# Kernel tuning notes

Hardware: AMD Instinct MI355X
Metric: run time of the kernel (lower is better)

The kernel has to match this reference:

```python
import jax, jax.numpy as jnp
import numpy as np

N_NODES = 50000
N_EDGES = 800000
D_IN = 16


def gcn_conv(x, edge_index, W, b, n_nodes):
    """PyG GCNConv: x' = D^{-1/2} (A + I) D^{-1/2} X W + b (add_self_loops=True)."""
    h = x @ W  # [N, d_out] - transform before propagate (small d => cheaper)
    src = jnp.concatenate([edge_index[0], jnp.arange(n_nodes)])  # add self-loops
    dst = jnp.concatenate([edge_index[1], jnp.arange(n_nodes)])
    deg = jax.ops.segment_sum(jnp.ones_like(dst, dtype=h.dtype), dst,
                              num_segments=n_nodes)  # in-degree incl. self-loop
    deg_inv_sqrt = jnp.where(deg > 0, jax.lax.rsqrt(deg), 0.0)
    norm = deg_inv_sqrt[src] * deg_inv_sqrt[dst]  # [E+N]
    msg = h[src] * norm[:, None]                  # gather + scale
    out = jax.ops.segment_sum(msg, dst, num_segments=n_nodes)  # scatter-add
    return out + b


def setup_inputs() -> dict:
    key = jax.random.key(0)
    ks = jax.random.split(key, 16)
    d = D_IN
    x = jax.random.normal(ks[0], (N_NODES, d), dtype=jnp.float32)
    edge_index = jax.random.randint(ks[1], (2, N_EDGES), 0, N_NODES, dtype=jnp.int64)

    def glorot(k, fan_in, fan_out):
        s = (6.0 / (fan_in + fan_out)) ** 0.5
        return jax.random.uniform(k, (fan_in, fan_out), jnp.float32, -s, s)

    return {
        "x": x,
        "edge_index": edge_index,
        "W1": glorot(ks[2], d, 2 * d),      "b1": jnp.zeros((2 * d,), jnp.float32),
        "W2": glorot(ks[3], 2 * d, 4 * d),  "b2": jnp.zeros((4 * d,), jnp.float32),
        "W3": glorot(ks[4], 4 * d, 8 * d),  "b3": jnp.zeros((8 * d,), jnp.float32),
        "Wl1": glorot(ks[5], 8 * d, 4 * d), "bl1": jnp.zeros((4 * d,), jnp.float32),
        "Wl2": glorot(ks[6], 4 * d, 2 * d), "bl2": jnp.zeros((2 * d,), jnp.float32),
        "Wl3": glorot(ks[7], 2 * d, d),     "bl3": jnp.zeros((d,), jnp.float32),
    }


def reference(x, edge_index, W1, b1, W2, b2, W3, b3, Wl1, bl1, Wl2, bl2, Wl3, bl3):
    n = x.shape[0]
    # note: original applies relu twice per conv; relu is idempotent
    out = jax.nn.relu(gcn_conv(x, edge_index, W1, b1, n))
    out = jax.nn.relu(gcn_conv(out, edge_index, W2, b2, n))
    out = jax.nn.relu(gcn_conv(out, edge_index, W3, b3, n))
    out = jax.nn.relu(out @ Wl1 + bl1)
    out = jax.nn.relu(out @ Wl2 + bl2)
    out = jax.nn.relu(out @ Wl3 + bl3)
    return out
```

## Files before the change

kernel.cpp:

```cpp
#include <hip/hip_runtime.h>

#define TPB 256
#define TE  2048
#define MAXB 6144

typedef _Float16 half_t;
typedef _Float16 half4 __attribute__((ext_vector_type(4)));
typedef _Float16 half8 __attribute__((ext_vector_type(8)));
typedef float float8v __attribute__((ext_vector_type(8)));

static inline int cdiv(int a, int b) { return (a + b - 1) / b; }


__global__ void k_zero_int(int* p, int n) {
    int i = blockIdx.x * blockDim.x + threadIdx.x;
    if (i < n) p[i] = 0;
}

__global__ void __launch_bounds__(TPB)
k_binscatter(const int* __restrict__ src, const int* __restrict__ dst,
             int* __restrict__ bcur, unsigned int* __restrict__ gbuf,
             int e, int nb) {
    __shared__ int lcnt[256], loffs[256], lcur[256], gres[256];
    __shared__ int ss[256];
    __shared__ unsigned int ldata[TE];
    const int tid = threadIdx.x;
    const int base = blockIdx.x * TE;
    const int cnt = min(TE, e - base);
    lcnt[tid] = 0;
    __syncthreads();

    unsigned int myv[TE / TPB];
    int myb[TE / TPB];
#pragma unroll
    for (int k = 0; k < TE / TPB; ++k) {
        int j = tid + k * TPB;
        if (j < cnt) {
            int d = dst[base + j], s = src[base + j];
            int b = d >> 8;
            myv[k] = ((unsigned)b << 24) | ((unsigned)(d & 255) << 16) | (unsigned)s;
            myb[k] = b;
            atomicAdd(&lcnt[b], 1);
        } else myb[k] = -1;
    }
    __syncthreads();
    {
        int v = lcnt[tid];
        ss[tid] = v;
        __syncthreads();
        for (int d = 1; d < 256; d <<= 1) {
            int x2 = (tid >= d) ? ss[tid - d] : 0;
            __syncthreads();
            ss[tid] += x2;
            __syncthreads();
        }
        loffs[tid] = ss[tid] - v;
        lcur[tid] = ss[tid] - v;
    }
    __syncthreads();
    if (tid < nb && lcnt[tid])
        gres[tid] = tid * MAXB + atomicAdd(&bcur[tid], lcnt[tid]);
#pragma unroll
    for (int k = 0; k < TE / TPB; ++k) {
        if (myb[k] >= 0) {
            int p = atomicAdd(&lcur[myb[k]], 1);
            ldata[p] = myv[k];
        }
    }
    __syncthreads();
    for (int j = tid; j < cnt; j += TPB) {
        unsigned int v = ldata[j];
        int b = v >> 24;
        gbuf[gres[b] + (j - loffs[b])] = v & 0xFFFFFFu;
    }
}

__global__ void __launch_bounds__(TPB)
k_csr(const unsigned int* __restrict__ gbuf, const int* __restrict__ bcur,
      const float* __restrict__ x, int* __restrict__ offs,
      unsigned short* __restrict__ nch, float* __restrict__ dinv,
      unsigned short* __restrict__ ssrc, half_t* __restrict__ G, int n, int nb) {
    __shared__ int ss[256], cnt[256], loffs2[256], lcur2[256], pcnt[256];
    __shared__ float sdinv[256];
    __shared__ unsigned short stage[MAXB];
    const int b = blockIdx.x;
    const int t = threadIdx.x;
    const int s0 = b * MAXB;
    const int m = bcur[b];

    cnt[t] = 0;
    __syncthreads();
    for (int j = t; j < m; j += TPB)
        atomicAdd(&cnt[(gbuf[s0 + j] >> 16) & 255], 1);
    __syncthreads();
    {
        int v = cnt[t];
        int pv = (v + 7) & ~7;
        pcnt[t] = pv;
        ss[t] = pv;
        __syncthreads();
        for (int d = 1; d < 256; d <<= 1) {
            int x2 = (t >= d) ? ss[t - d] : 0;
            __syncthreads();
            ss[t] += x2;
            __syncthreads();
        }
        loffs2[t] = ss[t] - pv;
        lcur2[t] = ss[t] - pv;
        float di = rsqrtf((float)v + 1.0f);
        sdinv[t] = di;
        int node = b * 256 + t;
        if (node < n) {
            offs[node] = s0 + loffs2[t];
            nch[node] = (unsigned short)(pv >> 3);
            dinv[node] = di;
        }
    }
    __syncthreads();
    for (int j = t; j < m; j += TPB) {
        unsigned int v = gbuf[s0 + j];
        int p = atomicAdd(&lcur2[(v >> 16) & 255], 1);
        stage[p] = (unsigned short)(v & 0xFFFFu);
    }
    __syncthreads();
    {
        int base2 = loffs2[t] + cnt[t], end2 = loffs2[t] + pcnt[t];
        for (int q = base2; q < end2; ++q) stage[q] = (unsigned short)n;
    }
    __syncthreads();
    const int tot = ss[255];
    for (int j = t; j < tot; j += TPB) ssrc[s0 + j] = stage[j];

    const int base = b * 256;
    const int cn = min(256, n - base);
    const float4* X4 = (const float4*)x;
    half4* G4 = (half4*)G;
    for (int j = t; j < cn * 4; j += TPB) {
        int nl = j >> 2, k4 = j & 3;
        float4 v = X4[(size_t)(base + nl) * 4 + k4];
        float d = sdinv[nl];
        half4 h;
        h.x = (half_t)(v.x * d); h.y = (half_t)(v.y * d);
        h.z = (half_t)(v.z * d); h.w = (half_t)(v.w * d);
        G4[(size_t)(base + nl) * 4 + k4] = h;
    }
    if (b == 0 && t < 4) G4[(size_t)n * 4 + t] = half4{0, 0, 0, 0};
}

template<int DI, int DO, int R, bool SCALE, bool OUT_HALF, bool WHALF, bool ZSENT>
__global__ void __launch_bounds__(TPB, 4)
k_conv(const int* __restrict__ offs, const unsigned short* __restrict__ nch,
       const unsigned short* __restrict__ ssrc,
       const half_t* __restrict__ G, const float* __restrict__ dinv,
       const float* __restrict__ W, const float* __restrict__ b,
       void* __restrict__ outp, int n) {
    constexpr int CT = DO / 4;
    constexpr int RT = TPB / CT;
    constexpr int TM = RT * R;
    constexpr int K4 = DI / 4;
    constexpr int PX = K4 + 1;
    constexpr int C  = DI / 8;
    static_assert(TM * C == TPB, "gather/gemm tile mismatch");
    __shared__ float4 sW4[WHALF ? 1 : DI * CT];
    __shared__ half4  sWh[WHALF ? DI * CT : 1];
    __shared__ float4 sX4[TM * PX];
    __shared__ int soffs[TM];
    __shared__ unsigned short snch[TM];
    const int tid = threadIdx.x;
    const int r0 = blockIdx.x * TM;

    const float4* Wg = (const float4*)W;
    for (int t = tid; t < DI * CT; t += TPB) {
        float4 w = Wg[t];
        if (WHALF) {
            half4 h;
            h.x = (half_t)w.x; h.y = (half_t)w.y;
            h.z = (half_t)w.z; h.w = (half_t)w.w;
            sWh[t] = h;
        } else {
            sW4[t] = w;
        }
    }
    if (tid < TM) {
        int row = r0 + tid;
        soffs[tid] = (row < n) ? offs[row] : 0;
        snch[tid] = (row < n) ? nch[row] : (unsigned short)0;
    }
    __syncthreads();

    {
        int lrow = tid / C;
        int gc = tid - lrow * C;
        int row = r0 + lrow;
        float8v acc;
#pragma unroll
        for (int q = 0; q < 8; ++q) acc[q] = 0.f;
        if (row < n) {
            const half8* Grow = (const half8*)G;
            const unsigned gcU = (unsigned)gc;
            half8 hs = Grow[(unsigned)row * C + gcU];
#pragma unroll
            for (int q = 0; q < 8; ++q) acc[q] = (float)hs[q];
            const int nchunks = snch[lrow];
            const uint4* sv = (const uint4*)(ssrc + soffs[lrow]);
            int k = 0;
            for (; k + 2 <= nchunks; k += 2) {
                uint4 pa = sv[k];
                uint4 pb = sv[k + 1];
                unsigned a0 = pa.x & 0xFFFFu, a1 = pa.x >> 16;
                unsigned a2 = pa.y & 0xFFFFu, a3 = pa.y >> 16;
                unsigned a4 = pa.z & 0xFFFFu, a5 = pa.z >> 16;
                unsigned a6 = pa.w & 0xFFFFu, a7 = pa.w >> 16;
                unsigned b0 = pb.x & 0xFFFFu, b1 = pb.x >> 16;
                unsigned b2 = pb.y & 0xFFFFu, b3 = pb.y >> 16;
                unsigned b4 = pb.z & 0xFFFFu, b5 = pb.z >> 16;
                unsigned b6 = pb.w & 0xFFFFu, b7 = pb.w >> 16;
                half8 ga0 = Grow[a0 * C + gcU];
                half8 ga1 = Grow[a1 * C + gcU];
                half8 ga2 = Grow[a2 * C + gcU];
                half8 ga3 = Grow[a3 * C + gcU];
                half8 ga4 = Grow[a4 * C + gcU];
                half8 ga5 = Grow[a5 * C + gcU];
                half8 ga6 = Grow[a6 * C + gcU];
                half8 ga7 = Grow[a7 * C + gcU];
                half8 gb0 = Grow[b0 * C + gcU];
                half8 gb1 = Grow[b1 * C + gcU];
                half8 gb2 = Grow[b2 * C + gcU];
                half8 gb3 = Grow[b3 * C + gcU];
                half8 gb4 = Grow[b4 * C + gcU];
                half8 gb5 = Grow[b5 * C + gcU];
                half8 gb6 = Grow[b6 * C + gcU];
                half8 gb7 = Grow[b7 * C + gcU];
#pragma unroll
                for (int q = 0; q < 8; ++q)
                    acc[q] += (((((float)ga0[q] + (float)ga1[q]) + ((float)ga2[q] + (float)ga3[q]))
                             +  (((float)ga4[q] + (float)ga5[q]) + ((float)ga6[q] + (float)ga7[q])))
                             + ((((float)gb0[q] + (float)gb1[q]) + ((float)gb2[q] + (float)gb3[q]))
                             +  (((float)gb4[q] + (float)gb5[q]) + ((float)gb6[q] + (float)gb7[q]))));
            }
            if (k < nchunks) {
                uint4 pk = sv[k];
                unsigned a0 = pk.x & 0xFFFFu, a1 = pk.x >> 16;
                unsigned a2 = pk.y & 0xFFFFu, a3 = pk.y >> 16;
                unsigned a4 = pk.z & 0xFFFFu, a5 = pk.z >> 16;
                unsigned a6 = pk.w & 0xFFFFu, a7 = pk.w >> 16;
                half8 g0 = Grow[a0 * C + gcU];
                half8 g1 = Grow[a1 * C + gcU];
                half8 g2 = Grow[a2 * C + gcU];
                half8 g3 = Grow[a3 * C + gcU];
                half8 g4 = Grow[a4 * C + gcU];
                half8 g5 = Grow[a5 * C + gcU];
                half8 g6 = Grow[a6 * C + gcU];
                half8 g7 = Grow[a7 * C + gcU];
#pragma unroll
                for (int q = 0; q < 8; ++q)
                    acc[q] += (((float)g0[q] + (float)g1[q]) + ((float)g2[q] + (float)g3[q]))
                            + (((float)g4[q] + (float)g5[q]) + ((float)g6[q] + (float)g7[q]));
            }
            float di = dinv[row];
#pragma unroll
            for (int q = 0; q < 8; ++q) acc[q] *= di;
        }
        sX4[lrow * PX + 2 * gc]     = make_float4(acc[0], acc[1], acc[2], acc[3]);
        sX4[lrow * PX + 2 * gc + 1] = make_float4(acc[4], acc[5], acc[6], acc[7]);
    }
    __syncthreads();

    const int c = tid & (CT - 1);
    const int rg = tid / CT;
    const int rbase = rg * R;
    float4 acc[R];
#pragma unroll
    for (int r = 0; r < R; ++r) acc[r] = make_float4(0.f, 0.f, 0.f, 0.f);

#pragma unroll 2
    for (int k4 = 0; k4 < K4; ++k4) {
        float4 xv[R];
#pragma unroll
        for (int r = 0; r < R; ++r) xv[r] = sX4[(rbase + r) * PX + k4];
#pragma unroll
        for (int kk = 0; kk < 4; ++kk) {
            float4 wv;
            if (WHALF) {
                half4 wh = sWh[(k4 * 4 + kk) * CT + c];
                wv = make_float4((float)wh.x, (float)wh.y, (float)wh.z, (float)wh.w);
            } else {
                wv = sW4[(k4 * 4 + kk) * CT + c];
            }
#pragma unroll
            for (int r = 0; r < R; ++r) {
                float xs = (kk == 0) ? xv[r].x : (kk == 1) ? xv[r].y
                         : (kk == 2) ? xv[r].z : xv[r].w;
                acc[r].x += xs * wv.x; acc[r].y += xs * wv.y;
                acc[r].z += xs * wv.z; acc[r].w += xs * wv.w;
            }
        }
    }

    float4 bc = ((const float4*)b)[c];
#pragma unroll
    for (int r = 0; r < R; ++r) {
        int row = r0 + rbase + r;
        if (row < n) {
            float4 o;
            o.x = fmaxf(acc[r].x + bc.x, 0.f);
            o.y = fmaxf(acc[r].y + bc.y, 0.f);
            o.z = fmaxf(acc[r].z + bc.z, 0.f);
            o.w = fmaxf(acc[r].w + bc.w, 0.f);
            if (SCALE) {
                float d = dinv[row];
                o.x *= d; o.y *= d; o.z *= d; o.w *= d;
            }
            if (OUT_HALF) {
                half4 h;
                h.x = (half_t)o.x; h.y = (half_t)o.y;
                h.z = (half_t)o.z; h.w = (half_t)o.w;
                ((half4*)outp)[(size_t)row * CT + c] = h;
            } else {
                ((float4*)outp)[(size_t)row * CT + c] = o;
            }
        }
    }
    if (ZSENT && OUT_HALF && blockIdx.x == 0 && tid < CT)
        ((half4*)outp)[(size_t)n * CT + tid] = half4{0, 0, 0, 0};
}

__global__ void __launch_bounds__(256, 3)
k_head(const half_t* __restrict__ X,
       const float* __restrict__ W1, const float* __restrict__ b1,
       const float* __restrict__ W2, const float* __restrict__ b2,
       const float* __restrict__ W3, const float* __restrict__ b3,
       float* __restrict__ out, int n) {
    __shared__ half_t hW1[128 * 64];
    __shared__ half_t hW2[64 * 32];
    __shared__ half_t hW3[32 * 16];
    __shared__ float h1[64 * 65];
    __shared__ float h2[64 * 33];
    const int tid = threadIdx.x;
    const int r0 = blockIdx.x * 64;

    for (int t = tid; t < 128 * 64; t += 256) hW1[t] = (half_t)W1[t];
    for (int t = tid; t < 64 * 32; t += 256) hW2[t] = (half_t)W2[t];
    for (int t = tid; t < 32 * 16; t += 256) hW3[t] = (half_t)W3[t];
    __syncthreads();

    {
        const int c4 = tid & 15;
        const int rowg = tid >> 4;
        const half8* Xr = (const half8*)X;
        float acc[4][4];
#pragma unroll
        for (int r = 0; r < 4; ++r)
#pragma unroll
            for (int j = 0; j < 4; ++j) acc[r][j] = 0.f;
        for (int k8 = 0; k8 < 16; ++k8) {
            half8 xh[4];
#pragma unroll
            for (int r = 0; r < 4; ++r) {
                int row = r0 + rowg * 4 + r;
                if (row < n) xh[r] = Xr[(size_t)row * 16 + k8];
                else { half8 z; for (int q = 0; q < 8; ++q) z[q] = (half_t)0.f; xh[r] = z; }
            }
#pragma unroll
            for (int q = 0; q < 8; ++q) {
                int k = k8 * 8 + q;
                half4 w = *(const half4*)&hW1[k * 64 + c4 * 4];
                float w0 = (float)w.x, w1 = (float)w.y, w2 = (float)w.z, w3 = (float)w.w;
#pragma unroll
                for (int r = 0; r < 4; ++r) {
                    float xs = (float)xh[r][q];
                    acc[r][0] += xs * w0; acc[r][1] += xs * w1;
                    acc[r][2] += xs * w2; acc[r][3] += xs * w3;
                }
            }
        }
        float4 bc = ((const float4*)b1)[c4];
#pragma unroll
        for (int r = 0; r < 4; ++r) {
            int rl = rowg * 4 + r;
            h1[rl * 65 + c4 * 4 + 0] = fmaxf(acc[r][0] + bc.x, 0.f);
            h1[rl * 65 + c4 * 4 + 1] = fmaxf(acc[r][1] + bc.y, 0.f);
            h1[rl * 65 + c4 * 4 + 2] = fmaxf(acc[r][2] + bc.z, 0.f);
            h1[rl * 65 + c4 * 4 + 3] = fmaxf(acc[r][3] + bc.w, 0.f);
        }
    }
    __syncthreads();

    {
        const int c4 = tid & 7;
        const int rowg = tid >> 3;
        float acc[2][4];
#pragma unroll
        for (int r = 0; r < 2; ++r)
#pragma unroll
            for (int j = 0; j < 4; ++j) acc[r][j] = 0.f;
#pragma unroll 4
        for (int k = 0; k < 64; ++k) {
            half4 w = *(const half4*)&hW2[k * 32 + c4 * 4];
            float w0 = (float)w.x, w1 = (float)w.y, w2 = (float)w.z, w3 = (float)w.w;
#pragma unroll
            for (int r = 0; r < 2; ++r) {
                float xs = h1[(rowg * 2 + r) * 65 + k];
                acc[r][0] += xs * w0; acc[r][1] += xs * w1;
                acc[r][2] += xs * w2; acc[r][3] += xs * w3;
            }
        }
        float4 bc = ((const float4*)b2)[c4];
#pragma unroll
        for (int r = 0; r < 2; ++r) {
            int rl = rowg * 2 + r;
            h2[rl * 33 + c4 * 4 + 0] = fmaxf(acc[r][0] + bc.x, 0.f);
            h2[rl * 33 + c4 * 4 + 1] = fmaxf(acc[r][1] + bc.y, 0.f);
            h2[rl * 33 + c4 * 4 + 2] = fmaxf(acc[r][2] + bc.z, 0.f);
            h2[rl * 33 + c4 * 4 + 3] = fmaxf(acc[r][3] + bc.w, 0.f);
        }
    }
    __syncthreads();

    {
        const int c4 = tid & 3;
        const int rl = tid >> 2;
        float a0 = 0.f, a1 = 0.f, a2 = 0.f, a3 = 0.f;
#pragma unroll 4
        for (int k = 0; k < 32; ++k) {
            half4 w = *(const half4*)&hW3[k * 16 + c4 * 4];
            float xs = h2[rl * 33 + k];
            a0 += xs * (float)w.x; a1 += xs * (float)w.y;
            a2 += xs * (float)w.z; a3 += xs * (float)w.w;
        }
        int row = r0 + rl;
        if (row < n) {
            float4 bc = ((const float4*)b3)[c4];
            float4 o;
            o.x = fmaxf(a0 + bc.x, 0.f);
            o.y = fmaxf(a1 + bc.y, 0.f);
            o.z = fmaxf(a2 + bc.z, 0.f);
            o.w = fmaxf(a3 + bc.w, 0.f);
            ((float4*)out)[(size_t)row * 4 + c4] = o;
        }
    }
}

extern "C" void kernel_launch(void* const* d_in, const int* in_sizes, int n_in,
                              void* d_out, int out_size, void* d_ws, size_t ws_size,
                              hipStream_t stream) {
    const float* x   = (const float*)d_in[0];
    const int*   ei  = (const int*)d_in[1];
    const float* W1  = (const float*)d_in[2];
    const float* bb1 = (const float*)d_in[3];
    const float* W2  = (const float*)d_in[4];
    const float* bb2 = (const float*)d_in[5];
    const float* W3  = (const float*)d_in[6];
    const float* bb3 = (const float*)d_in[7];
    const float* Wl1 = (const float*)d_in[8];
    const float* bl1 = (const float*)d_in[9];
    const float* Wl2 = (const float*)d_in[10];
    const float* bl2 = (const float*)d_in[11];
    const float* Wl3 = (const float*)d_in[12];
    const float* bl3 = (const float*)d_in[13];
    float* out = (float*)d_out;

    const int n = in_sizes[0] / 16;
    const int e = in_sizes[1] / 2;
    const int* src = ei;
    const int* dst = ei + e;
    const int nb = cdiv(n, 256);

    char* p = (char*)d_ws;
    auto alloc = [&](size_t bytes) {
        char* r = p;
        p += (bytes + 255) & ~(size_t)255;
        return r;
    };
    float*          dinv = (float*)         alloc((size_t)n * 4);
    int*            offs = (int*)           alloc((size_t)n * 4);
    unsigned short* nch  = (unsigned short*)alloc((size_t)n * 2);
    int*            bcur = (int*)           alloc(256 * 4);
    unsigned int*   gbuf = (unsigned int*)  alloc((size_t)nb * MAXB * 4);
    unsigned short* ssrc = (unsigned short*)alloc((size_t)nb * MAXB * 2);
    half_t*         H1   = (half_t*)        alloc((size_t)(n + 1) * 64 * 2);
    half_t*         H2   = (half_t*)        alloc((size_t)(n + 1) * 32 * 2);
    half_t*         X3h  = (half_t*)        alloc((size_t)n * 128 * 2);

    k_zero_int<<<1, 256, 0, stream>>>(bcur, 256);
    k_binscatter<<<cdiv(e, TE), TPB, 0, stream>>>(src, dst, bcur, gbuf, e, nb);
    k_csr<<<nb, TPB, 0, stream>>>(gbuf, bcur, x, offs, nch, dinv, ssrc, H1, n, nb);

    k_conv<16, 32, 4, true, true, false, true><<<cdiv(n, 128), TPB, 0, stream>>>(
        offs, nch, ssrc, H1, dinv, W1, bb1, H2, n);
    k_conv<32, 64, 4, true, true, false, true><<<cdiv(n, 64), TPB, 0, stream>>>(
        offs, nch, ssrc, H2, dinv, W2, bb2, H1, n);
    k_conv<64, 128, 4, false, true, true, false><<<cdiv(n, 32), TPB, 0, stream>>>(
        offs, nch, ssrc, H1, dinv, W3, bb3, X3h, n);

    k_head<<<cdiv(n, 64), 256, 0, stream>>>(X3h, Wl1, bl1, Wl2, bl2, Wl3, bl3, out, n);
}
```

Measured before the change: 198.9 us.

## Fuse all stages into a persistent megakernel with software grid barriers

Replaces the seven separate kernel launches (zeroing, bin scatter, CSR build, three convolutions, MLP head) with one persistent kernel of 512 blocks. Each block grid-strides over tiles in every phase, and the phases are separated by an atomic-counter grid barrier. Shared memory is reused through a union of per-phase layouts. The aim is to remove launch gaps and tail effects. In exchange it adds barrier spin cost, needs all 512 blocks to be co-resident (the barrier has a timeout fallback), and the union's size may cut occupancy.

```diff
diff --git a/kernel.cpp b/kernel.cpp
--- a/kernel.cpp
+++ b/kernel.cpp
@@ -3,157 +3,203 @@
 #define TPB 256
 #define TE  2048
 #define MAXB 6144
+#define GRID 512
 
 typedef _Float16 half_t;
 typedef _Float16 half4 __attribute__((ext_vector_type(4)));
 typedef _Float16 half8 __attribute__((ext_vector_type(8)));
 typedef float float8v __attribute__((ext_vector_type(8)));
 
-static inline int cdiv(int a, int b) { return (a + b - 1) / b; }
-
-
-__global__ void k_zero_int(int* p, int n) {
-    int i = blockIdx.x * blockDim.x + threadIdx.x;
-    if (i < n) p[i] = 0;
-}
-
-__global__ void __launch_bounds__(TPB)
-k_binscatter(const int* __restrict__ src, const int* __restrict__ dst,
-             int* __restrict__ bcur, unsigned int* __restrict__ gbuf,
-             int e, int nb) {
-    __shared__ int lcnt[256], loffs[256], lcur[256], gres[256];
-    __shared__ int ss[256];
-    __shared__ unsigned int ldata[TE];
-    const int tid = threadIdx.x;
-    const int base = blockIdx.x * TE;
-    const int cnt = min(TE, e - base);
-    lcnt[tid] = 0;
+__host__ __device__ static inline constexpr int cdiv(int a, int b) { return (a + b - 1) / b; }
+
+struct SBin {
+    int lcnt[256], loffs[256], lcur[256], gres[256], ss[256];
+    unsigned int ldata[TE];
+};
+struct SCsr {
+    int ss[256], cnt[256], loffs2[256], lcur2[256], pcnt[256];
+    float sdinv[256];
+    unsigned short stage[MAXB];
+};
+template<int DI, int DO, int R, bool WHALF>
+struct SConv {
+    static constexpr int CT = DO / 4;
+    static constexpr int TM = (TPB / CT) * R;
+    static constexpr int PX = DI / 4 + 1;
+    float4 sW4[WHALF ? 1 : DI * CT];
+    half4  sWh[WHALF ? DI * CT : 1];
+    float4 sX4[TM * PX];
+    int soffs[TM];
+    unsigned short snch[TM];
+};
+struct SHead {
+    half_t hW1[128 * 64], hW2[64 * 32], hW3[32 * 16];
+    float h1[64 * 65], h2[64 * 33];
+};
+union SMemAll {
+    SBin b;
+    SCsr c;
+    SConv<16, 32, 4, false>  c1;
+    SConv<32, 64, 4, false>  c2;
+    SConv<64, 128, 4, true>  c3;
+    SHead h;
+};
+
+__device__ __forceinline__ void gridbar(unsigned int* cnt, unsigned int* gen, unsigned int nb) {
     __syncthreads();
-
-    unsigned int myv[TE / TPB];
-    int myb[TE / TPB];
-#pragma unroll
-    for (int k = 0; k < TE / TPB; ++k) {
-        int j = tid + k * TPB;
-        if (j < cnt) {
-            int d = dst[base + j], s = src[base + j];
-            int b = d >> 8;
-            myv[k] = ((unsigned)b << 24) | ((unsigned)(d & 255) << 16) | (unsigned)s;
-            myb[k] = b;
-            atomicAdd(&lcnt[b], 1);
-        } else myb[k] = -1;
+    if (threadIdx.x == 0) {
+        unsigned int g = __hip_atomic_load(gen, __ATOMIC_RELAXED, __HIP_MEMORY_SCOPE_AGENT);
+        __threadfence();
+        unsigned int a = __hip_atomic_fetch_add(cnt, 1u, __ATOMIC_ACQ_REL, __HIP_MEMORY_SCOPE_AGENT);
+        if (a == nb - 1u) {
+            __hip_atomic_store(cnt, 0u, __ATOMIC_RELAXED, __HIP_MEMORY_SCOPE_AGENT);
+            __hip_atomic_fetch_add(gen, 1u, __ATOMIC_RELEASE, __HIP_MEMORY_SCOPE_AGENT);
+        } else {
+            unsigned int spins = 0;
+            while (__hip_atomic_load(gen, __ATOMIC_ACQUIRE, __HIP_MEMORY_SCOPE_AGENT) == g) {
+                __builtin_amdgcn_s_sleep(2);
+                if (++spins > 3000000u) break;
+            }
+        }
+        __threadfence();
     }
     __syncthreads();
-    {
-        int v = lcnt[tid];
-        ss[tid] = v;
-        __syncthreads();
-        for (int d = 1; d < 256; d <<= 1) {
-            int x2 = (tid >= d) ? ss[tid - d] : 0;
+}
+
+__device__ __forceinline__ void phase_binscatter(SBin& L, const int* __restrict__ src,
+        const int* __restrict__ dst, int* __restrict__ bcur,
+        unsigned int* __restrict__ gbuf, int e, int nb) {
+    const int tid = threadIdx.x;
+    const int ntiles = cdiv(e, TE);
+    for (int bb = blockIdx.x; bb < ntiles; bb += gridDim.x) {
+        const int base = bb * TE;
+        const int cnt = min(TE, e - base);
+        L.lcnt[tid] = 0;
+        __syncthreads();
+        unsigned int myv[TE / TPB];
+        int myb[TE / TPB];
+#pragma unroll
+        for (int k = 0; k < TE / TPB; ++k) {
+            int j = tid + k * TPB;
+            if (j < cnt) {
+                int d = dst[base + j], s = src[base + j];
+                int b = d >> 8;
+                myv[k] = ((unsigned)b << 24) | ((unsigned)(d & 255) << 16) | (unsigned)s;
+                myb[k] = b;
+                atomicAdd(&L.lcnt[b], 1);
+            } else myb[k] = -1;
+        }
+        __syncthreads();
+        {
+            int v = L.lcnt[tid];
+            L.ss[tid] = v;
             __syncthreads();
-            ss[tid] += x2;
+            for (int d = 1; d < 256; d <<= 1) {
+                int x2 = (tid >= d) ? L.ss[tid - d] : 0;
+                __syncthreads();
+                L.ss[tid] += x2;
+                __syncthreads();
+            }
+            L.loffs[tid] = L.ss[tid] - v;
+            L.lcur[tid] = L.ss[tid] - v;
+        }
+        __syncthreads();
+        if (tid < nb && L.lcnt[tid])
+            L.gres[tid] = tid * MAXB + atomicAdd(&bcur[tid], L.lcnt[tid]);
+#pragma unroll
+        for (int k = 0; k < TE / TPB; ++k) {
+            if (myb[k] >= 0) {
+                int p = atomicAdd(&L.lcur[myb[k]], 1);
+                L.ldata[p] = myv[k];
+            }
+        }
+        __syncthreads();
+        for (int j = tid; j < cnt; j += TPB) {
+            unsigned int v = L.ldata[j];
+            int b = v >> 24;
+            gbuf[L.gres[b] + (j - L.loffs[b])] = v & 0xFFFFFFu;
+        }
+        __syncthreads();
+    }
+}
+
+__device__ __forceinline__ void phase_csr(SCsr& L, const unsigned int* __restrict__ gbuf,
+        const int* __restrict__ bcur, const float* __restrict__ x,
+        int* __restrict__ offs, unsigned short* __restrict__ nch,
+        float* __restrict__ dinv, unsigned short* __restrict__ ssrc,
+        half_t* __restrict__ G, int n, int nb) {
+    const int t = threadIdx.x;
+    for (int bb = blockIdx.x; bb < nb; bb += gridDim.x) {
+        const int s0 = bb * MAXB;
+        const int m = bcur[bb];
+        L.cnt[t] = 0;
+        __syncthreads();
+        for (int j = t; j < m; j += TPB)
+            atomicAdd(&L.cnt[(gbuf[s0 + j] >> 16) & 255], 1);
+        __syncthreads();
+        {
+            int v = L.cnt[t];
+            int pv = (v + 7) & ~7;
+            L.pcnt[t] = pv;
+            L.ss[t] = pv;
             __syncthreads();
-        }
-        loffs[tid] = ss[tid] - v;
-        lcur[tid] = ss[tid] - v;
+            for (int d = 1; d < 256; d <<= 1) {
+                int x2 = (t >= d) ? L.ss[t - d] : 0;
+                __syncthreads();
+                L.ss[t] += x2;
+                __syncthreads();
+            }
+            L.loffs2[t] = L.ss[t] - pv;
+            L.lcur2[t] = L.ss[t] - pv;
+            float di = rsqrtf((float)v + 1.0f);
+            L.sdinv[t] = di;
+            int node = bb * 256 + t;
+            if (node < n) {
+                offs[node] = s0 + L.loffs2[t];
+                nch[node] = (unsigned short)(pv >> 3);
+                dinv[node] = di;
+            }
+        }
+        __syncthreads();
+        for (int j = t; j < m; j += TPB) {
+            unsigned int v = gbuf[s0 + j];
+            int p = atomicAdd(&L.lcur2[(v >> 16) & 255], 1);
+            L.stage[p] = (unsigned short)(v & 0xFFFFu);
+        }
+        __syncthreads();
+        {
+            int base2 = L.loffs2[t] + L.cnt[t], end2 = L.loffs2[t] + L.pcnt[t];
+            for (int q = base2; q < end2; ++q) L.stage[q] = (unsigned short)n;
+        }
+        __syncthreads();
+        const int tot = L.ss[255];
+        for (int j = t; j < tot; j += TPB) ssrc[s0 + j] = L.stage[j];
+
+        const int base = bb * 256;
+        const int cn = min(256, n - base);
+        const float4* X4 = (const float4*)x;
+        half4* G4 = (half4*)G;
+        for (int j = t; j < cn * 4; j += TPB) {
+            int nl = j >> 2, k4 = j & 3;
+            float4 v = X4[(size_t)(base + nl) * 4 + k4];
+            float d = L.sdinv[nl];
+            half4 h;
+            h.x = (half_t)(v.x * d); h.y = (half_t)(v.y * d);
+            h.z = (half_t)(v.z * d); h.w = (half_t)(v.w * d);
+            G4[(size_t)(base + nl) * 4 + k4] = h;
+        }
+        if (bb == 0 && t < 4) G4[(size_t)n * 4 + t] = half4{0, 0, 0, 0};
+        __syncthreads();
     }
-    __syncthreads();
-    if (tid < nb && lcnt[tid])
-        gres[tid] = tid * MAXB + atomicAdd(&bcur[tid], lcnt[tid]);
-#pragma unroll
-    for (int k = 0; k < TE / TPB; ++k) {
-        if (myb[k] >= 0) {
-            int p = atomicAdd(&lcur[myb[k]], 1);
-            ldata[p] = myv[k];
-        }
-    }
-    __syncthreads();
-    for (int j = tid; j < cnt; j += TPB) {
-        unsigned int v = ldata[j];
-        int b = v >> 24;
-        gbuf[gres[b] + (j - loffs[b])] = v & 0xFFFFFFu;
-    }
-}
-
-__global__ void __launch_bounds__(TPB)
-k_csr(const unsigned int* __restrict__ gbuf, const int* __restrict__ bcur,
-      const float* __restrict__ x, int* __restrict__ offs,
-      unsigned short* __restrict__ nch, float* __restrict__ dinv,
-      unsigned short* __restrict__ ssrc, half_t* __restrict__ G, int n, int nb) {
-    __shared__ int ss[256], cnt[256], loffs2[256], lcur2[256], pcnt[256];
-    __shared__ float sdinv[256];
-    __shared__ unsigned short stage[MAXB];
-    const int b = blockIdx.x;
-    const int t = threadIdx.x;
-    const int s0 = b * MAXB;
-    const int m = bcur[b];
-
-    cnt[t] = 0;
-    __syncthreads();
-    for (int j = t; j < m; j += TPB)
-        atomicAdd(&cnt[(gbuf[s0 + j] >> 16) & 255], 1);
-    __syncthreads();
-    {
-        int v = cnt[t];
-        int pv = (v + 7) & ~7;
-        pcnt[t] = pv;
-        ss[t] = pv;
-        __syncthreads();
-        for (int d = 1; d < 256; d <<= 1) {
-            int x2 = (t >= d) ? ss[t - d] : 0;
-            __syncthreads();
-            ss[t] += x2;
-            __syncthreads();
-        }
-        loffs2[t] = ss[t] - pv;
-        lcur2[t] = ss[t] - pv;
-        float di = rsqrtf((float)v + 1.0f);
-        sdinv[t] = di;
-        int node = b * 256 + t;
-        if (node < n) {
-            offs[node] = s0 + loffs2[t];
-            nch[node] = (unsigned short)(pv >> 3);
-            dinv[node] = di;
-        }
-    }
-    __syncthreads();
-    for (int j = t; j < m; j += TPB) {
-        unsigned int v = gbuf[s0 + j];
-        int p = atomicAdd(&lcur2[(v >> 16) & 255], 1);
-        stage[p] = (unsigned short)(v & 0xFFFFu);
-    }
-    __syncthreads();
-    {
-        int base2 = loffs2[t] + cnt[t], end2 = loffs2[t] + pcnt[t];
-        for (int q = base2; q < end2; ++q) stage[q] = (unsigned short)n;
-    }
-    __syncthreads();
-    const int tot = ss[255];
-    for (int j = t; j < tot; j += TPB) ssrc[s0 + j] = stage[j];
-
-    const int base = b * 256;
-    const int cn = min(256, n - base);
-    const float4* X4 = (const float4*)x;
-    half4* G4 = (half4*)G;
-    for (int j = t; j < cn * 4; j += TPB) {
-        int nl = j >> 2, k4 = j & 3;
-        float4 v = X4[(size_t)(base + nl) * 4 + k4];
-        float d = sdinv[nl];
-        half4 h;
-        h.x = (half_t)(v.x * d); h.y = (half_t)(v.y * d);
-        h.z = (half_t)(v.z * d); h.w = (half_t)(v.w * d);
-        G4[(size_t)(base + nl) * 4 + k4] = h;
-    }
-    if (b == 0 && t < 4) G4[(size_t)n * 4 + t] = half4{0, 0, 0, 0};
-}
-
-template<int DI, int DO, int R, bool SCALE, bool OUT_HALF, bool WHALF, bool ZSENT>
-__global__ void __launch_bounds__(TPB, 4)
-k_conv(const int* __restrict__ offs, const unsigned short* __restrict__ nch,
-       const unsigned short* __restrict__ ssrc,
-       const half_t* __restrict__ G, const float* __restrict__ dinv,
-       const float* __restrict__ W, const float* __restrict__ b,
-       void* __restrict__ outp, int n) {
+}
+
+template<int DI, int DO, int R, bool SCALE, bool OUT_HALF, bool WHALF, bool ZSENT, typename SM>
+__device__ __forceinline__ void phase_conv(SM& S,
+        const int* __restrict__ offs, const unsigned short* __restrict__ nch,
+        const unsigned short* __restrict__ ssrc,
+        const half_t* __restrict__ G, const float* __restrict__ dinv,
+        const float* __restrict__ W, const float* __restrict__ b,
+        void* __restrict__ outp, int n) {
     constexpr int CT = DO / 4;
     constexpr int RT = TPB / CT;
     constexpr int TM = RT * R;
@@ -161,13 +207,8 @@
     constexpr int PX = K4 + 1;
     constexpr int C  = DI / 8;
     static_assert(TM * C == TPB, "gather/gemm tile mismatch");
-    __shared__ float4 sW4[WHALF ? 1 : DI * CT];
-    __shared__ half4  sWh[WHALF ? DI * CT : 1];
-    __shared__ float4 sX4[TM * PX];
-    __shared__ int soffs[TM];
-    __shared__ unsigned short snch[TM];
     const int tid = threadIdx.x;
-    const int r0 = blockIdx.x * TM;
+    const int ntiles = cdiv(n, TM);
 
     const float4* Wg = (const float4*)W;
     for (int t = tid; t < DI * CT; t += TPB) {
@@ -176,269 +217,305 @@
             half4 h;
             h.x = (half_t)w.x; h.y = (half_t)w.y;
             h.z = (half_t)w.z; h.w = (half_t)w.w;
-            sWh[t] = h;
+            S.sWh[t] = h;
         } else {
-            sW4[t] = w;
+            S.sW4[t] = w;
         }
     }
-    if (tid < TM) {
-        int row = r0 + tid;
-        soffs[tid] = (row < n) ? offs[row] : 0;
-        snch[tid] = (row < n) ? nch[row] : (unsigned short)0;
+
+    for (int bb = blockIdx.x; bb < ntiles; bb += gridDim.x) {
+        const int r0 = bb * TM;
+        if (tid < TM) {
+            int row = r0 + tid;
+            S.soffs[tid] = (row < n) ? offs[row] : 0;
+            S.snch[tid] = (row < n) ? nch[row] : (unsigned short)0;
+        }
+        __syncthreads();
+
+        {
+            int lrow = tid / C;
+            int gc = tid - lrow * C;
+            int row = r0 + lrow;
+            float8v acc;
+#pragma unroll
+            for (int q = 0; q < 8; ++q) acc[q] = 0.f;
+            if (row < n) {
+                const half8* Grow = (const half8*)G;
+                const unsigned gcU = (unsigned)gc;
+                half8 hs = Grow[(unsigned)row * C + gcU];
+#pragma unroll
+                for (int q = 0; q < 8; ++q) acc[q] = (float)hs[q];
+                const int nchunks = S.snch[lrow];
+                const uint4* sv = (const uint4*)(ssrc + S.soffs[lrow]);
+                int k = 0;
+                for (; k + 2 <= nchunks; k += 2) {
+                    uint4 pa = sv[k];
+                    uint4 pb = sv[k + 1];
+                    unsigned a0 = pa.x & 0xFFFFu, a1 = pa.x >> 16;
+                    unsigned a2 = pa.y & 0xFFFFu, a3 = pa.y >> 16;
+                    unsigned a4 = pa.z & 0xFFFFu, a5 = pa.z >> 16;
+                    unsigned a6 = pa.w & 0xFFFFu, a7 = pa.w >> 16;
+                    unsigned b0 = pb.x & 0xFFFFu, b1 = pb.x >> 16;
+                    unsigned b2 = pb.y & 0xFFFFu, b3 = pb.y >> 16;
+                    unsigned b4 = pb.z & 0xFFFFu, b5 = pb.z >> 16;
+                    unsigned b6 = pb.w & 0xFFFFu, b7 = pb.w >> 16;
+                    half8 ga0 = Grow[a0 * C + gcU];
+                    half8 ga1 = Grow[a1 * C + gcU];
+                    half8 ga2 = Grow[a2 * C + gcU];
+                    half8 ga3 = Grow[a3 * C + gcU];
+                    half8 ga4 = Grow[a4 * C + gcU];
+                    half8 ga5 = Grow[a5 * C + gcU];
+                    half8 ga6 = Grow[a6 * C + gcU];
+                    half8 ga7 = Grow[a7 * C + gcU];
+                    half8 gb0 = Grow[b0 * C + gcU];
+                    half8 gb1 = Grow[b1 * C + gcU];
+                    half8 gb2 = Grow[b2 * C + gcU];
+                    half8 gb3 = Grow[b3 * C + gcU];
+                    half8 gb4 = Grow[b4 * C + gcU];
+                    half8 gb5 = Grow[b5 * C + gcU];
+                    half8 gb6 = Grow[b6 * C + gcU];
+                    half8 gb7 = Grow[b7 * C + gcU];
+#pragma unroll
+                    for (int q = 0; q < 8; ++q)
+                        acc[q] += (((((float)ga0[q] + (float)ga1[q]) + ((float)ga2[q] + (float)ga3[q]))
+                                 +  (((float)ga4[q] + (float)ga5[q]) + ((float)ga6[q] + (float)ga7[q])))
+                                 + ((((float)gb0[q] + (float)gb1[q]) + ((float)gb2[q] + (float)gb3[q]))
+                                 +  (((float)gb4[q] + (float)gb5[q]) + ((float)gb6[q] + (float)gb7[q]))));
+                }
+                if (k < nchunks) {
+                    uint4 pk = sv[k];
+                    unsigned a0 = pk.x & 0xFFFFu, a1 = pk.x >> 16;
+                    unsigned a2 = pk.y & 0xFFFFu, a3 = pk.y >> 16;
+                    unsigned a4 = pk.z & 0xFFFFu, a5 = pk.z >> 16;
+                    unsigned a6 = pk.w & 0xFFFFu, a7 = pk.w >> 16;
+                    half8 g0 = Grow[a0 * C + gcU];
+                    half8 g1 = Grow[a1 * C + gcU];
+                    half8 g2 = Grow[a2 * C + gcU];
+                    half8 g3 = Grow[a3 * C + gcU];
+                    half8 g4 = Grow[a4 * C + gcU];
+                    half8 g5 = Grow[a5 * C + gcU];
+                    half8 g6 = Grow[a6 * C + gcU];
+                    half8 g7 = Grow[a7 * C + gcU];
+#pragma unroll
+                    for (int q = 0; q < 8; ++q)
+                        acc[q] += (((float)g0[q] + (float)g1[q]) + ((float)g2[q] + (float)g3[q]))
+                                + (((float)g4[q] + (float)g5[q]) + ((float)g6[q] + (float)g7[q]));
+                }
+                float di = dinv[row];
+#pragma unroll
+                for (int q = 0; q < 8; ++q) acc[q] *= di;
+            }
+            S.sX4[lrow * PX + 2 * gc]     = make_float4(acc[0], acc[1], acc[2], acc[3]);
+            S.sX4[lrow * PX + 2 * gc + 1] = make_float4(acc[4], acc[5], acc[6], acc[7]);
+        }
+        __syncthreads();
+
+        {
+            const int c = tid & (CT - 1);
+            const int rg = tid / CT;
+            const int rbase = rg * R;
+            float4 acc[R];
+#pragma unroll
+            for (int r = 0; r < R; ++r) acc[r] = make_float4(0.f, 0.f, 0.f, 0.f);
+
+#pragma unroll 2
+            for (int k4 = 0; k4 < K4; ++k4) {
+                float4 xv[R];
+#pragma unroll
+                for (int r = 0; r < R; ++r) xv[r] = S.sX4[(rbase + r) * PX + k4];
+#pragma unroll
+                for (int kk = 0; kk < 4; ++kk) {
+                    float4 wv;
+                    if (WHALF) {
+                        half4 wh = S.sWh[(k4 * 4 + kk) * CT + c];
+                        wv = make_float4((float)wh.x, (float)wh.y, (float)wh.z, (float)wh.w);
+                    } else {
+                        wv = S.sW4[(k4 * 4 + kk) * CT + c];
+                    }
+#pragma unroll
+                    for (int r = 0; r < R; ++r) {
+                        float xs = (kk == 0) ? xv[r].x : (kk == 1) ? xv[r].y
+                                 : (kk == 2) ? xv[r].z : xv[r].w;
+                        acc[r].x += xs * wv.x; acc[r].y += xs * wv.y;
+                        acc[r].z += xs * wv.z; acc[r].w += xs * wv.w;
+                    }
+                }
+            }
+
+            float4 bc = ((const float4*)b)[c];
+#pragma unroll
+            for (int r = 0; r < R; ++r) {
+                int row = r0 + rbase + r;
+                if (row < n) {
+                    float4 o;
+                    o.x = fmaxf(acc[r].x + bc.x, 0.f);
+                    o.y = fmaxf(acc[r].y + bc.y, 0.f);
+                    o.z = fmaxf(acc[r].z + bc.z, 0.f);
+                    o.w = fmaxf(acc[r].w + bc.w, 0.f);
+                    if (SCALE) {
+                        float d = dinv[row];
+                        o.x *= d; o.y *= d; o.z *= d; o.w *= d;
+                    }
+                    if (OUT_HALF) {
+                        half4 h;
+                        h.x = (half_t)o.x; h.y = (half_t)o.y;
+                        h.z = (half_t)o.z; h.w = (half_t)o.w;
+                        ((half4*)outp)[(size_t)row * CT + c] = h;
+                    } else {
+                        ((float4*)outp)[(size_t)row * CT + c] = o;
+                    }
+                }
+            }
+        }
+        if (ZSENT && OUT_HALF && bb == 0 && tid < CT)
+            ((half4*)outp)[(size_t)n * CT + tid] = half4{0, 0, 0, 0};
+        __syncthreads();
     }
+}
+
+__device__ __forceinline__ void phase_head(SHead& L, const half_t* __restrict__ X,
+        const float* __restrict__ W1, const float* __restrict__ b1,
+        const float* __restrict__ W2, const float* __restrict__ b2,
+        const float* __restrict__ W3, const float* __restrict__ b3,
+        float* __restrict__ out, int n) {
+    const int tid = threadIdx.x;
+    const int ntiles = cdiv(n, 64);
+
+    for (int t = tid; t < 128 * 64; t += 256) L.hW1[t] = (half_t)W1[t];
+    for (int t = tid; t < 64 * 32; t += 256) L.hW2[t] = (half_t)W2[t];
+    for (int t = tid; t < 32 * 16; t += 256) L.hW3[t] = (half_t)W3[t];
     __syncthreads();
 
-    {
-        int lrow = tid / C;
-        int gc = tid - lrow * C;
-        int row = r0 + lrow;
-        float8v acc;
-#pragma unroll
-        for (int q = 0; q < 8; ++q) acc[q] = 0.f;
-        if (row < n) {
-            const half8* Grow = (const half8*)G;
-            const unsigned gcU = (unsigned)gc;
-            half8 hs = Grow[(unsigned)row * C + gcU];
-#pragma unroll
-            for (int q = 0; q < 8; ++q) acc[q] = (float)hs[q];
-            const int nchunks = snch[lrow];
-            const uint4* sv = (const uint4*)(ssrc + soffs[lrow]);
-            int k = 0;
-            for (; k + 2 <= nchunks; k += 2) {
-                uint4 pa = sv[k];
-                uint4 pb = sv[k + 1];
-                unsigned a0 = pa.x & 0xFFFFu, a1 = pa.x >> 16;
-                unsigned a2 = pa.y & 0xFFFFu, a3 = pa.y >> 16;
-                unsigned a4 = pa.z & 0xFFFFu, a5 = pa.z >> 16;
-                unsigned a6 = pa.w & 0xFFFFu, a7 = pa.w >> 16;
-                unsigned b0 = pb.x & 0xFFFFu, b1 = pb.x >> 16;
-                unsigned b2 = pb.y & 0xFFFFu, b3 = pb.y >> 16;
-                unsigned b4 = pb.z & 0xFFFFu, b5 = pb.z >> 16;
-                unsigned b6 = pb.w & 0xFFFFu, b7 = pb.w >> 16;
-                half8 ga0 = Grow[a0 * C + gcU];
-                half8 ga1 = Grow[a1 * C + gcU];
-                half8 ga2 = Grow[a2 * C + gcU];
-                half8 ga3 = Grow[a3 * C + gcU];
-                half8 ga4 = Grow[a4 * C + gcU];
-                half8 ga5 = Grow[a5 * C + gcU];
-                half8 ga6 = Grow[a6 * C + gcU];
-                half8 ga7 = Grow[a7 * C + gcU];
-                half8 gb0 = Grow[b0 * C + gcU];
-                half8 gb1 = Grow[b1 * C + gcU];
-                half8 gb2 = Grow[b2 * C + gcU];
-                half8 gb3 = Grow[b3 * C + gcU];
-                half8 gb4 = Grow[b4 * C + gcU];
-                half8 gb5 = Grow[b5 * C + gcU];
-                half8 gb6 = Grow[b6 * C + gcU];
-                half8 gb7 = Grow[b7 * C + gcU];
-#pragma unroll
-                for (int q = 0; q < 8; ++q)
-                    acc[q] += (((((float)ga0[q] + (float)ga1[q]) + ((float)ga2[q] + (float)ga3[q]))
-                             +  (((float)ga4[q] + (float)ga5[q]) + ((float)ga6[q] + (float)ga7[q])))
-                             + ((((float)gb0[q] + (float)gb1[q]) + ((float)gb2[q] + (float)gb3[q]))
-                             +  (((float)gb4[q] + (float)gb5[q]) + ((float)gb6[q] + (float)gb7[q]))));
-            }
-            if (k < nchunks) {
-                uint4 pk = sv[k];
-                unsigned a0 = pk.x & 0xFFFFu, a1 = pk.x >> 16;
-                unsigned a2 = pk.y & 0xFFFFu, a3 = pk.y >> 16;
-                unsigned a4 = pk.z & 0xFFFFu, a5 = pk.z >> 16;
-                unsigned a6 = pk.w & 0xFFFFu, a7 = pk.w >> 16;
-                half8 g0 = Grow[a0 * C + gcU];
-                half8 g1 = Grow[a1 * C + gcU];
-                half8 g2 = Grow[a2 * C + gcU];
-                half8 g3 = Grow[a3 * C + gcU];
-                half8 g4 = Grow[a4 * C + gcU];
-                half8 g5 = Grow[a5 * C + gcU];
-                half8 g6 = Grow[a6 * C + gcU];
-                half8 g7 = Grow[a7 * C + gcU];
-#pragma unroll
-                for (int q = 0; q < 8; ++q)
-                    acc[q] += (((float)g0[q] + (float)g1[q]) + ((float)g2[q] + (float)g3[q]))
-                            + (((float)g4[q] + (float)g5[q]) + ((float)g6[q] + (float)g7[q]));
-            }
-            float di = dinv[row];
-#pragma unroll
-            for (int q = 0; q < 8; ++q) acc[q] *= di;
-        }
-        sX4[lrow * PX + 2 * gc]     = make_float4(acc[0], acc[1], acc[2], acc[3]);
-        sX4[lrow * PX + 2 * gc + 1] = make_float4(acc[4], acc[5], acc[6], acc[7]);
+    for (int bb = blockIdx.x; bb < ntiles; bb += gridDim.x) {
+        const int r0 = bb * 64;
+        {
+            const int c4 = tid & 15;
+            const int rowg = tid >> 4;
+            const half8* Xr = (const half8*)X;
+            float acc[4][4];
+#pragma unroll
+            for (int r = 0; r < 4; ++r)
+#pragma unroll
+                for (int j = 0; j < 4; ++j) acc[r][j] = 0.f;
+            for (int k8 = 0; k8 < 16; ++k8) {
+                half8 xh[4];
+#pragma unroll
+                for (int r = 0; r < 4; ++r) {
+                    int row = r0 + rowg * 4 + r;
+                    if (row < n) xh[r] = Xr[(size_t)row * 16 + k8];
+                    else { half8 z; for (int q = 0; q < 8; ++q) z[q] = (half_t)0.f; xh[r] = z; }
+                }
+#pragma unroll
+                for (int q = 0; q < 8; ++q) {
+                    int k = k8 * 8 + q;
+                    half4 w = *(const half4*)&L.hW1[k * 64 + c4 * 4];
+                    float w0 = (float)w.x, w1 = (float)w.y, w2 = (float)w.z, w3 = (float)w.w;
+#pragma unroll
+                    for (int r = 0; r < 4; ++r) {
+                        float xs = (float)xh[r][q];
+                        acc[r][0] += xs * w0; acc[r][1] += xs * w1;
+                        acc[r][2] += xs * w2; acc[r][3] += xs * w3;
+                    }
+                }
+            }
+            float4 bc = ((const float4*)b1)[c4];
+#pragma unroll
+            for (int r = 0; r < 4; ++r) {
+                int rl = rowg * 4 + r;
+                L.h1[rl * 65 + c4 * 4 + 0] = fmaxf(acc[r][0] + bc.x, 0.f);
+                L.h1[rl * 65 + c4 * 4 + 1] = fmaxf(acc[r][1] + bc.y, 0.f);
+                L.h1[rl * 65 + c4 * 4 + 2] = fmaxf(acc[r][2] + bc.z, 0.f);
+                L.h1[rl * 65 + c4 * 4 + 3] = fmaxf(acc[r][3] + bc.w, 0.f);
+            }
+        }
+        __syncthreads();
+
+        {
+            const int c4 = tid & 7;
+            const int rowg = tid >> 3;
+            float acc[2][4];
+#pragma unroll
+            for (int r = 0; r < 2; ++r)
+#pragma unroll
+                for (int j = 0; j < 4; ++j) acc[r][j] = 0.f;
+#pragma unroll 4
+            for (int k = 0; k < 64; ++k) {
+                half4 w = *(const half4*)&L.hW2[k * 32 + c4 * 4];
+                float w0 = (float)w.x, w1 = (float)w.y, w2 = (float)w.z, w3 = (float)w.w;
+#pragma unroll
+                for (int r = 0; r < 2; ++r) {
+                    float xs = L.h1[(rowg * 2 + r) * 65 + k];
+                    acc[r][0] += xs * w0; acc[r][1] += xs * w1;
+                    acc[r][2] += xs * w2; acc[r][3] += xs * w3;
+                }
+            }
+            float4 bc = ((const float4*)b2)[c4];
+#pragma unroll
+            for (int r = 0; r < 2; ++r) {
+                int rl = rowg * 2 + r;
+                L.h2[rl * 33 + c4 * 4 + 0] = fmaxf(acc[r][0] + bc.x, 0.f);
+                L.h2[rl * 33 + c4 * 4 + 1] = fmaxf(acc[r][1] + bc.y, 0.f);
+                L.h2[rl * 33 + c4 * 4 + 2] = fmaxf(acc[r][2] + bc.z, 0.f);
+                L.h2[rl * 33 + c4 * 4 + 3] = fmaxf(acc[r][3] + bc.w, 0.f);
+            }
+        }
+        __syncthreads();
+
+        {
+            const int c4 = tid & 3;
+            const int rl = tid >> 2;
+            float a0 = 0.f, a1 = 0.f, a2 = 0.f, a3 = 0.f;
+#pragma unroll 4
+            for (int k = 0; k < 32; ++k) {
+                half4 w = *(const half4*)&L.hW3[k * 16 + c4 * 4];
+                float xs = L.h2[rl * 33 + k];
+                a0 += xs * (float)w.x; a1 += xs * (float)w.y;
+                a2 += xs * (float)w.z; a3 += xs * (float)w.w;
+            }
+            int row = r0 + rl;
+            if (row < n) {
+                float4 bc = ((const float4*)b3)[c4];
+                float4 o;
+                o.x = fmaxf(a0 + bc.x, 0.f);
+                o.y = fmaxf(a1 + bc.y, 0.f);
+                o.z = fmaxf(a2 + bc.z, 0.f);
+                o.w = fmaxf(a3 + bc.w, 0.f);
+                ((float4*)out)[(size_t)row * 4 + c4] = o;
+            }
+        }
+        __syncthreads();
     }
-    __syncthreads();
-
-    const int c = tid & (CT - 1);
-    const int rg = tid / CT;
-    const int rbase = rg * R;
-    float4 acc[R];
-#pragma unroll
-    for (int r = 0; r < R; ++r) acc[r] = make_float4(0.f, 0.f, 0.f, 0.f);
-
-#pragma unroll 2
-    for (int k4 = 0; k4 < K4; ++k4) {
-        float4 xv[R];
-#pragma unroll
-        for (int r = 0; r < R; ++r) xv[r] = sX4[(rbase + r) * PX + k4];
-#pragma unroll
-        for (int kk = 0; kk < 4; ++kk) {
-            float4 wv;
-            if (WHALF) {
-                half4 wh = sWh[(k4 * 4 + kk) * CT + c];
-                wv = make_float4((float)wh.x, (float)wh.y, (float)wh.z, (float)wh.w);
-            } else {
-                wv = sW4[(k4 * 4 + kk) * CT + c];
-            }
-#pragma unroll
-            for (int r = 0; r < R; ++r) {
-                float xs = (kk == 0) ? xv[r].x : (kk == 1) ? xv[r].y
-                         : (kk == 2) ? xv[r].z : xv[r].w;
-                acc[r].x += xs * wv.x; acc[r].y += xs * wv.y;
-                acc[r].z += xs * wv.z; acc[r].w += xs * wv.w;
-            }
-        }
-    }
-
-    float4 bc = ((const float4*)b)[c];
-#pragma unroll
-    for (int r = 0; r < R; ++r) {
-        int row = r0 + rbase + r;
-        if (row < n) {
-            float4 o;
-            o.x = fmaxf(acc[r].x + bc.x, 0.f);
-            o.y = fmaxf(acc[r].y + bc.y, 0.f);
-            o.z = fmaxf(acc[r].z + bc.z, 0.f);
-            o.w = fmaxf(acc[r].w + bc.w, 0.f);
-            if (SCALE) {
-                float d = dinv[row];
-                o.x *= d; o.y *= d; o.z *= d; o.w *= d;
-            }
-            if (OUT_HALF) {
-                half4 h;
-                h.x = (half_t)o.x; h.y = (half_t)o.y;
-                h.z = (half_t)o.z; h.w = (half_t)o.w;
-                ((half4*)outp)[(size_t)row * CT + c] = h;
-            } else {
-                ((float4*)outp)[(size_t)row * CT + c] = o;
-            }
-        }
-    }
-    if (ZSENT && OUT_HALF && blockIdx.x == 0 && tid < CT)
-        ((half4*)outp)[(size_t)n * CT + tid] = half4{0, 0, 0, 0};
-}
-
-__global__ void __launch_bounds__(256, 3)
-k_head(const half_t* __restrict__ X,
+}
+
+__global__ void __launch_bounds__(TPB, 2)
+k_mega(const int* __restrict__ src, const int* __restrict__ dst,
+       const float* __restrict__ x,
        const float* __restrict__ W1, const float* __restrict__ b1,
        const float* __restrict__ W2, const float* __restrict__ b2,
        const float* __restrict__ W3, const float* __restrict__ b3,
-       float* __restrict__ out, int n) {
-    __shared__ half_t hW1[128 * 64];
-    __shared__ half_t hW2[64 * 32];
-    __shared__ half_t hW3[32 * 16];
-    __shared__ float h1[64 * 65];
-    __shared__ float h2[64 * 33];
-    const int tid = threadIdx.x;
-    const int r0 = blockIdx.x * 64;
-
-    for (int t = tid; t < 128 * 64; t += 256) hW1[t] = (half_t)W1[t];
-    for (int t = tid; t < 64 * 32; t += 256) hW2[t] = (half_t)W2[t];
-    for (int t = tid; t < 32 * 16; t += 256) hW3[t] = (half_t)W3[t];
-    __syncthreads();
-
-    {
-        const int c4 = tid & 15;
-        const int rowg = tid >> 4;
-        const half8* Xr = (const half8*)X;
-        float acc[4][4];
-#pragma unroll
-        for (int r = 0; r < 4; ++r)
-#pragma unroll
-            for (int j = 0; j < 4; ++j) acc[r][j] = 0.f;
-        for (int k8 = 0; k8 < 16; ++k8) {
-            half8 xh[4];
-#pragma unroll
-            for (int r = 0; r < 4; ++r) {
-                int row = r0 + rowg * 4 + r;
-                if (row < n) xh[r] = Xr[(size_t)row * 16 + k8];
-                else { half8 z; for (int q = 0; q < 8; ++q) z[q] = (half_t)0.f; xh[r] = z; }
-            }
-#pragma unroll
-            for (int q = 0; q < 8; ++q) {
-                int k = k8 * 8 + q;
-                half4 w = *(const half4*)&hW1[k * 64 + c4 * 4];
-                float w0 = (float)w.x, w1 = (float)w.y, w2 = (float)w.z, w3 = (float)w.w;
-#pragma unroll
-                for (int r = 0; r < 4; ++r) {
-                    float xs = (float)xh[r][q];
-                    acc[r][0] += xs * w0; acc[r][1] += xs * w1;
-                    acc[r][2] += xs * w2; acc[r][3] += xs * w3;
-                }
-            }
-        }
-        float4 bc = ((const float4*)b1)[c4];
-#pragma unroll
-        for (int r = 0; r < 4; ++r) {
-            int rl = rowg * 4 + r;
-            h1[rl * 65 + c4 * 4 + 0] = fmaxf(acc[r][0] + bc.x, 0.f);
-            h1[rl * 65 + c4 * 4 + 1] = fmaxf(acc[r][1] + bc.y, 0.f);
-            h1[rl * 65 + c4 * 4 + 2] = fmaxf(acc[r][2] + bc.z, 0.f);
-            h1[rl * 65 + c4 * 4 + 3] = fmaxf(acc[r][3] + bc.w, 0.f);
-        }
-    }
-    __syncthreads();
-
-    {
-        const int c4 = tid & 7;
-        const int rowg = tid >> 3;
-        float acc[2][4];
-#pragma unroll
-        for (int r = 0; r < 2; ++r)
-#pragma unroll
-            for (int j = 0; j < 4; ++j) acc[r][j] = 0.f;
-#pragma unroll 4
-        for (int k = 0; k < 64; ++k) {
-            half4 w = *(const half4*)&hW2[k * 32 + c4 * 4];
-            float w0 = (float)w.x, w1 = (float)w.y, w2 = (float)w.z, w3 = (float)w.w;
-#pragma unroll
-            for (int r = 0; r < 2; ++r) {
-                float xs = h1[(rowg * 2 + r) * 65 + k];
-                acc[r][0] += xs * w0; acc[r][1] += xs * w1;
-                acc[r][2] += xs * w2; acc[r][3] += xs * w3;
-            }
-        }
-        float4 bc = ((const float4*)b2)[c4];
-#pragma unroll
-        for (int r = 0; r < 2; ++r) {
-            int rl = rowg * 2 + r;
-            h2[rl * 33 + c4 * 4 + 0] = fmaxf(acc[r][0] + bc.x, 0.f);
-            h2[rl * 33 + c4 * 4 + 1] = fmaxf(acc[r][1] + bc.y, 0.f);
-            h2[rl * 33 + c4 * 4 + 2] = fmaxf(acc[r][2] + bc.z, 0.f);
-            h2[rl * 33 + c4 * 4 + 3] = fmaxf(acc[r][3] + bc.w, 0.f);
-        }
-    }
-    __syncthreads();
-
-    {
-        const int c4 = tid & 3;
-        const int rl = tid >> 2;
-        float a0 = 0.f, a1 = 0.f, a2 = 0.f, a3 = 0.f;
-#pragma unroll 4
-        for (int k = 0; k < 32; ++k) {
-            half4 w = *(const half4*)&hW3[k * 16 + c4 * 4];
-            float xs = h2[rl * 33 + k];
-            a0 += xs * (float)w.x; a1 += xs * (float)w.y;
-            a2 += xs * (float)w.z; a3 += xs * (float)w.w;
-        }
-        int row = r0 + rl;
-        if (row < n) {
-            float4 bc = ((const float4*)b3)[c4];
-            float4 o;
-            o.x = fmaxf(a0 + bc.x, 0.f);
-            o.y = fmaxf(a1 + bc.y, 0.f);
-            o.z = fmaxf(a2 + bc.z, 0.f);
-            o.w = fmaxf(a3 + bc.w, 0.f);
-            ((float4*)out)[(size_t)row * 4 + c4] = o;
-        }
-    }
+       const float* __restrict__ Wl1, const float* __restrict__ bl1,
+       const float* __restrict__ Wl2, const float* __restrict__ bl2,
+       const float* __restrict__ Wl3, const float* __restrict__ bl3,
+       int* __restrict__ bcur, unsigned int* __restrict__ gcnt, unsigned int* __restrict__ ggen,
+       unsigned int* __restrict__ gbuf, int* __restrict__ offs,
+       unsigned short* __restrict__ nch, float* __restrict__ dinv,
+       unsigned short* __restrict__ ssrc,
+       half_t* __restrict__ H1, half_t* __restrict__ H2, half_t* __restrict__ X3h,
+       float* __restrict__ out, int n, int e, int nb) {
+    __shared__ SMemAll S;
+    const unsigned int NB = gridDim.x;
+
+    phase_binscatter(S.b, src, dst, bcur, gbuf, e, nb);
+    gridbar(gcnt, ggen, NB);
+    phase_csr(S.c, gbuf, bcur, x, offs, nch, dinv, ssrc, H1, n, nb);
+    gridbar(gcnt, ggen, NB);
+    phase_conv<16, 32, 4, true, true, false, true>(S.c1, offs, nch, ssrc, H1, dinv, W1, b1, H2, n);
+    gridbar(gcnt, ggen, NB);
+    phase_conv<32, 64, 4, true, true, false, true>(S.c2, offs, nch, ssrc, H2, dinv, W2, b2, H1, n);
+    gridbar(gcnt, ggen, NB);
+    phase_conv<64, 128, 4, false, true, true, false>(S.c3, offs, nch, ssrc, H1, dinv, W3, b3, X3h, n);
+    gridbar(gcnt, ggen, NB);
+    phase_head(S.h, X3h, Wl1, bl1, Wl2, bl2, Wl3, bl3, out, n);
 }
 
 extern "C" void kernel_launch(void* const* d_in, const int* in_sizes, int n_in,
@@ -472,26 +549,23 @@
         p += (bytes + 255) & ~(size_t)255;
         return r;
     };
+    char*           ctrl = alloc(4096);
+    int*            bcur = (int*)ctrl;
+    unsigned int*   gcnt = (unsigned int*)(ctrl + 1024);
+    unsigned int*   ggen = (unsigned int*)(ctrl + 1088);
     float*          dinv = (float*)         alloc((size_t)n * 4);
     int*            offs = (int*)           alloc((size_t)n * 4);
     unsigned short* nch  = (unsigned short*)alloc((size_t)n * 2);
-    int*            bcur = (int*)           alloc(256 * 4);
     unsigned int*   gbuf = (unsigned int*)  alloc((size_t)nb * MAXB * 4);
     unsigned short* ssrc = (unsigned short*)alloc((size_t)nb * MAXB * 2);
     half_t*         H1   = (half_t*)        alloc((size_t)(n + 1) * 64 * 2);
     half_t*         H2   = (half_t*)        alloc((size_t)(n + 1) * 32 * 2);
     half_t*         X3h  = (half_t*)        alloc((size_t)n * 128 * 2);
 
-    k_zero_int<<<1, 256, 0, stream>>>(bcur, 256);
-    k_binscatter<<<cdiv(e, TE), TPB, 0, stream>>>(src, dst, bcur, gbuf, e, nb);
-    k_csr<<<nb, TPB, 0, stream>>>(gbuf, bcur, x, offs, nch, dinv, ssrc, H1, n, nb);
-
-    k_conv<16, 32, 4, true, true, false, true><<<cdiv(n, 128), TPB, 0, stream>>>(
-        offs, nch, ssrc, H1, dinv, W1, bb1, H2, n);
-    k_conv<32, 64, 4, true, true, false, true><<<cdiv(n, 64), TPB, 0, stream>>>(
-        offs, nch, ssrc, H2, dinv, W2, bb2, H1, n);
-    k_conv<64, 128, 4, false, true, true, false><<<cdiv(n, 32), TPB, 0, stream>>>(
-        offs, nch, ssrc, H1, dinv, W3, bb3, X3h, n);
-
-    k_head<<<cdiv(n, 64), 256, 0, stream>>>(X3h, Wl1, bl1, Wl2, bl2, Wl3, bl3, out, n);
-}
+    hipMemsetAsync(ctrl, 0, 4096, stream);
+    k_mega<<<GRID, TPB, 0, stream>>>(
+        src, dst, x, W1, bb1, W2, bb2, W3, bb3,
+        Wl1, bl1, Wl2, bl2, Wl3, bl3,
+        bcur, gcnt, ggen, gbuf, offs, nch, dinv, ssrc,
+        H1, H2, X3h, out, n, e, nb);
+}
```

New measurement: 729.9 us. +267.1%, slower.
